# Kernel optimization log

Measured on AMD Instinct MI355X. Metric: run time of the kernel, lower is better.

## Reference

```python
import jax, jax.numpy as jnp
import numpy as np

N = 100000      # nodes
E = 1_000_000   # edges (avg degree ~10)
D_IN = 64
HID = 64
N_CLS = 32


def setup_inputs() -> dict:
    key = jax.random.key(0)
    ks = jax.random.split(key, 9)
    x = jax.random.normal(ks[0], (N, D_IN), dtype=jnp.float32)
    edge_index = jax.random.randint(ks[1], (2, E), 0, N, dtype=jnp.int32)
    s_in = 1.0 / np.sqrt(D_IN)
    s_h = 1.0 / np.sqrt(HID)
    W1 = jax.random.normal(ks[2], (D_IN, HID), dtype=jnp.float32) * s_in
    b1 = jnp.zeros((HID,), dtype=jnp.float32)
    W2 = jax.random.normal(ks[3], (HID, HID), dtype=jnp.float32) * s_h
    b2 = jnp.zeros((HID,), dtype=jnp.float32)
    Wl = jax.random.normal(ks[4], (HID, N_CLS), dtype=jnp.float32) * s_h
    bl = jnp.zeros((N_CLS,), dtype=jnp.float32)
    return {"x": x, "edge_index": edge_index,
            "W1": W1, "b1": b1, "W2": W2, "b2": b2, "Wl": Wl, "bl": bl}


def reference(x, edge_index, W1, b1, W2, b2, Wl, bl):
    # GCNConv default: add self-loops, symmetric normalization D^-1/2 (A+I) D^-1/2
    loop = jnp.arange(N, dtype=edge_index.dtype)
    src = jnp.concatenate([edge_index[0], loop])  # [E+N]
    dst = jnp.concatenate([edge_index[1], loop])  # [E+N]

    deg = jax.ops.segment_sum(jnp.ones_like(dst, dtype=jnp.float32), dst,
                              num_segments=N)              # [N]
    dinv = jnp.where(deg > 0, jax.lax.rsqrt(deg), 0.0)      # D^-1/2
    norm = dinv[src] * dinv[dst]                            # [E+N]

    def gcn_conv(h, W, b):
        h = h @ W                                           # [N, F_out]
        msg = h[src] * norm[:, None]                        # gather + scale
        return jax.ops.segment_sum(msg, dst, num_segments=N) + b

    h = jax.nn.relu(gcn_conv(x, W1, b1))
    h = jax.nn.relu(gcn_conv(h, W2, b2))
    return h @ Wl + bl
```

## Files before the change

### kernel.cpp

```cpp
#include <hip/hip_runtime.h>
#include <hip/hip_fp16.h>
#include <math.h>


#define TPB    256
#define TPB1   1024
#define EBLKS  256
#define BSH    7
#define BNODES (1 << BSH)

__global__ __launch_bounds__(TPB1)
void k_p1hist(const int* __restrict__ dst, int* __restrict__ OFS,
              int E, int CH, int NBC) {
    __shared__ int h[1024];
    int tid = threadIdx.x, b = blockIdx.x;
    h[tid] = 0;
    __syncthreads();
    int beg = b * CH, end = min(E, beg + CH);
    if (beg < end) {
        int nfull = (end - beg) & ~3;
        for (int i = beg + tid * 4; i < beg + nfull; i += TPB1 * 4) {
            int4 d = *(const int4*)&dst[i];
            atomicAdd(&h[d.x >> BSH], 1);
            atomicAdd(&h[d.y >> BSH], 1);
            atomicAdd(&h[d.z >> BSH], 1);
            atomicAdd(&h[d.w >> BSH], 1);
        }
        if (tid < (end - beg) - nfull)
            atomicAdd(&h[dst[beg + nfull + tid] >> BSH], 1);
    }
    __syncthreads();
    for (int c = tid; c < NBC; c += TPB1) OFS[c * EBLKS + b] = h[c];
}

__global__ __launch_bounds__(TPB)
void k_scanA(const int* __restrict__ OFS, int* __restrict__ bsum, int total) {
    __shared__ int s[TPB];
    int tid = threadIdx.x;
    int i0  = blockIdx.x * 1024 + tid * 4;
    int t = 0;
#pragma unroll
    for (int k = 0; k < 4; ++k) {
        int i = i0 + k;
        t += (i < total) ? OFS[i] : 0;
    }
    s[tid] = t;
    __syncthreads();
    for (int off = TPB / 2; off > 0; off >>= 1) {
        if (tid < off) s[tid] += s[tid + off];
        __syncthreads();
    }
    if (tid == 0) bsum[blockIdx.x] = s[0];
}

__global__ __launch_bounds__(TPB)
void k_scanC(int* __restrict__ OFS, const int* __restrict__ bsum, int total) {
    __shared__ int s[TPB];
    __shared__ int pfx;
    int tid = threadIdx.x;
    if (tid < 64) {
        int v = 0;
        for (int j = tid; j < (int)blockIdx.x; j += 64) v += bsum[j];
#pragma unroll
        for (int off = 1; off < 64; off <<= 1) v += __shfl_xor(v, off);
        if (tid == 0) pfx = v;
    }
    int i0 = blockIdx.x * 1024 + tid * 4;
    int v[4];
#pragma unroll
    for (int k = 0; k < 4; ++k) {
        int i = i0 + k;
        v[k] = (i < total) ? OFS[i] : 0;
    }
    int tsum = v[0] + v[1] + v[2] + v[3];
    s[tid] = tsum;
    __syncthreads();
    for (int off = 1; off < TPB; off <<= 1) {
        int x = (tid >= off) ? s[tid - off] : 0;
        __syncthreads();
        s[tid] += x;
        __syncthreads();
    }
    int base = pfx + (s[tid] - tsum);
#pragma unroll
    for (int k = 0; k < 4; ++k) {
        int i = i0 + k;
        if (i < total) {
            OFS[i] = base;
            base += v[k];
        }
    }
}

__global__ __launch_bounds__(TPB1)
void k_p1scatter(const int* __restrict__ src, const int* __restrict__ dst,
                 const int* __restrict__ OFS, int* __restrict__ ebuf,
                 int E, int CH, int NBC) {
    __shared__ int cur[1024];
    int tid = threadIdx.x, b = blockIdx.x;
    for (int c = tid; c < NBC; c += TPB1) cur[c] = OFS[c * EBLKS + b];
    __syncthreads();
    int beg = b * CH, end = min(E, beg + CH);
    if (beg >= end) return;
    int nfull = (end - beg) & ~3;
    for (int i = beg + tid * 4; i < beg + nfull; i += TPB1 * 4) {
        int4 s4 = *(const int4*)&src[i];
        int4 d4 = *(const int4*)&dst[i];
        int p0 = atomicAdd(&cur[d4.x >> BSH], 1);
        int p1 = atomicAdd(&cur[d4.y >> BSH], 1);
        int p2 = atomicAdd(&cur[d4.z >> BSH], 1);
        int p3 = atomicAdd(&cur[d4.w >> BSH], 1);
        ebuf[p0] = (s4.x << BSH) | (d4.x & (BNODES - 1));
        ebuf[p1] = (s4.y << BSH) | (d4.y & (BNODES - 1));
        ebuf[p2] = (s4.z << BSH) | (d4.z & (BNODES - 1));
        ebuf[p3] = (s4.w << BSH) | (d4.w & (BNODES - 1));
    }
    if (tid < (end - beg) - nfull) {
        int i = beg + nfull + tid;
        int d = dst[i];
        int p = atomicAdd(&cur[d >> BSH], 1);
        ebuf[p] = (src[i] << BSH) | (d & (BNODES - 1));
    }
}

__global__ __launch_bounds__(TPB)
void k_p2(const int* __restrict__ ebuf, const int* __restrict__ OFS,
          int* __restrict__ row_ptr, float* __restrict__ dinv,
          int* __restrict__ colw, int N, int E, int NBC) {
    __shared__ int cnt[BNODES];
    __shared__ int ofs[BNODES];
    __shared__ int s1[TPB];
    int tid = threadIdx.x, c = blockIdx.x;
    int beg = OFS[c * EBLKS];
    int end = (c == NBC - 1) ? E : OFS[(c + 1) * EBLKS];
    if (tid < BNODES) cnt[tid] = 0;
    __syncthreads();
    for (int i = beg + tid; i < end; i += TPB)
        atomicAdd(&cnt[ebuf[i] & (BNODES - 1)], 1);
    __syncthreads();
    int a = (tid < BNODES) ? cnt[tid] : 0;
    s1[tid] = a;
    __syncthreads();
    for (int off = 1; off < TPB; off <<= 1) {
        int x = (tid >= off) ? s1[tid - off] : 0;
        __syncthreads();
        s1[tid] += x;
        __syncthreads();
    }
    int ex = s1[tid] - a;
    if (tid < BNODES) {
        int node = (c << BSH) + tid;
        ofs[tid] = beg + ex;
        if (node < N) {
            row_ptr[node] = beg + ex;
            dinv[node]    = rsqrtf((float)(a + 1));
        }
        cnt[tid] = 0;
    }
    if (c == NBC - 1 && tid == 0) row_ptr[N] = E;
    __syncthreads();
    for (int i0 = beg + tid; i0 < end; i0 += TPB * 4) {
        int sv[4], dl[4], pos[4];
        int have = 0;
#pragma unroll
        for (int k = 0; k < 4; ++k) {
            int i = i0 + k * TPB;
            if (i < end) {
                int e = ebuf[i];
                sv[k] = e >> BSH;
                dl[k] = e & (BNODES - 1);
                have = k + 1;
            }
        }
#pragma unroll
        for (int k = 0; k < 4; ++k) {
            if (k < have) {
                int r  = atomicAdd(&cnt[dl[k]], 1);
                pos[k] = ofs[dl[k]] + r;
            }
        }
#pragma unroll
        for (int k = 0; k < 4; ++k)
            if (k < have) colw[pos[k]] = sv[k];
    }
}

template <int F, bool FINAL, bool HIN>
__launch_bounds__(256)
__global__ void k_mm(const void* __restrict__ in, const float* __restrict__ W,
                     const float* __restrict__ bias, const float* __restrict__ dinv,
                     void* __restrict__ out, int n) {
    __shared__ float in_s[64 * 68];
    __shared__ float w_s[64 * F];

    const int tid  = threadIdx.x;
    const int row0 = blockIdx.x * 64;

    for (int i4 = tid; i4 < (64 * F) / 4; i4 += 256)
        ((float4*)w_s)[i4] = ((const float4*)W)[i4];

    if constexpr (HIN) {
        for (int idx = tid; idx < 64 * 8; idx += 256) {
            int r  = idx >> 3;
            int c8 = idx & 7;
            uint4 u = make_uint4(0u, 0u, 0u, 0u);
            if (row0 + r < n)
                u = *(const uint4*)((const __half*)in + (size_t)(row0 + r) * 64 + c8 * 8);
            float2 f0 = __half22float2(*(__half2*)&u.x);
            float2 f1 = __half22float2(*(__half2*)&u.y);
            float2 f2 = __half22float2(*(__half2*)&u.z);
            float2 f3 = __half22float2(*(__half2*)&u.w);
            float* o = &in_s[r * 68 + c8 * 8];
            *(float4*)&o[0] = make_float4(f0.x, f0.y, f1.x, f1.y);
            *(float4*)&o[4] = make_float4(f2.x, f2.y, f3.x, f3.y);
        }
    } else {
        for (int idx = tid; idx < 64 * 16; idx += 256) {
            int r  = idx >> 4;
            int c4 = idx & 15;
            float4 v;
            if (row0 + r < n)
                v = *(const float4*)((const float*)in + (size_t)(row0 + r) * 64 + c4 * 4);
            else
                v = make_float4(0.f, 0.f, 0.f, 0.f);
            *(float4*)&in_s[r * 68 + c4 * 4] = v;
        }
    }
    __syncthreads();

    constexpr int CPT = F / 16;
    const int tx = tid & 15;
    const int ty = tid >> 4;

    float acc[4][CPT];
#pragma unroll
    for (int r = 0; r < 4; ++r)
#pragma unroll
        for (int c = 0; c < CPT; ++c) acc[r][c] = 0.f;

#pragma unroll 4
    for (int k = 0; k < 64; ++k) {
        float b[CPT];
#pragma unroll
        for (int c = 0; c < CPT; ++c) b[c] = w_s[k * F + tx * CPT + c];
#pragma unroll
        for (int r = 0; r < 4; ++r) {
            float a = in_s[(ty * 4 + r) * 68 + k];
#pragma unroll
            for (int c = 0; c < CPT; ++c) acc[r][c] = fmaf(a, b[c], acc[r][c]);
        }
    }

#pragma unroll
    for (int r = 0; r < 4; ++r) {
        int row = row0 + ty * 4 + r;
        if (row >= n) continue;
        if constexpr (FINAL) {
#pragma unroll
            for (int c = 0; c < CPT; ++c) {
                int col = tx * CPT + c;
                ((float*)out)[(size_t)row * F + col] = acc[r][c] + bias[col];
            }
        } else {
            float dd = dinv[row];
            __half2 p0 = __floats2half2_rn(acc[r][0] * dd, acc[r][1] * dd);
            __half2 p1 = __floats2half2_rn(acc[r][2] * dd, acc[r][3] * dd);
            uint2 u = make_uint2(*(unsigned*)&p0, *(unsigned*)&p1);
            *(uint2*)((__half*)out + (size_t)row * 64 + tx * 4) = u;
        }
    }
    if constexpr (!FINAL) {
        if (blockIdx.x == 0 && tid < 16)
            *(uint2*)((__half*)out + (size_t)n * 64 + tid * 4) = make_uint2(0u, 0u);
    }
}

__global__ __launch_bounds__(256)
void k_gather(const int* __restrict__ row_ptr, const int* __restrict__ colw,
              const float* __restrict__ dinv, const float* __restrict__ bias,
              const __half* __restrict__ t, __half* __restrict__ agg, int N) {
    int tid  = threadIdx.x;
    int wv   = tid >> 6;
    int lane = tid & 63;
    int g = lane >> 3;
    int p = lane & 7;
    int d = blockIdx.x * 32 + wv * 8 + g;

    int beg = 0, end = 0;
    if (d < N) { beg = row_ptr[d]; end = row_ptr[d + 1]; }

    float acc[8];
#pragma unroll
    for (int k = 0; k < 8; ++k) acc[k] = 0.f;

    for (int e = beg; e < end; e += 4) {
        int s0 = colw[e];
        int s1 = (e + 1 < end) ? colw[e + 1] : N;
        int s2 = (e + 2 < end) ? colw[e + 2] : N;
        int s3 = (e + 3 < end) ? colw[e + 3] : N;
        uint4 a0 = *(const uint4*)(t + (size_t)s0 * 64 + p * 8);
        uint4 a1 = *(const uint4*)(t + (size_t)s1 * 64 + p * 8);
        uint4 a2 = *(const uint4*)(t + (size_t)s2 * 64 + p * 8);
        uint4 a3 = *(const uint4*)(t + (size_t)s3 * 64 + p * 8);
        float2 f;
        f = __half22float2(*(__half2*)&a0.x); acc[0] += f.x; acc[1] += f.y;
        f = __half22float2(*(__half2*)&a0.y); acc[2] += f.x; acc[3] += f.y;
        f = __half22float2(*(__half2*)&a0.z); acc[4] += f.x; acc[5] += f.y;
        f = __half22float2(*(__half2*)&a0.w); acc[6] += f.x; acc[7] += f.y;
        f = __half22float2(*(__half2*)&a1.x); acc[0] += f.x; acc[1] += f.y;
        f = __half22float2(*(__half2*)&a1.y); acc[2] += f.x; acc[3] += f.y;
        f = __half22float2(*(__half2*)&a1.z); acc[4] += f.x; acc[5] += f.y;
        f = __half22float2(*(__half2*)&a1.w); acc[6] += f.x; acc[7] += f.y;
        f = __half22float2(*(__half2*)&a2.x); acc[0] += f.x; acc[1] += f.y;
        f = __half22float2(*(__half2*)&a2.y); acc[2] += f.x; acc[3] += f.y;
        f = __half22float2(*(__half2*)&a2.z); acc[4] += f.x; acc[5] += f.y;
        f = __half22float2(*(__half2*)&a2.w); acc[6] += f.x; acc[7] += f.y;
        f = __half22float2(*(__half2*)&a3.x); acc[0] += f.x; acc[1] += f.y;
        f = __half22float2(*(__half2*)&a3.y); acc[2] += f.x; acc[3] += f.y;
        f = __half22float2(*(__half2*)&a3.z); acc[4] += f.x; acc[5] += f.y;
        f = __half22float2(*(__half2*)&a3.w); acc[6] += f.x; acc[7] += f.y;
    }

    if (d < N) {
        float dd = dinv[d];
        uint4 a = *(const uint4*)(t + (size_t)d * 64 + p * 8);
        float4 b0 = *(const float4*)&bias[p * 8];
        float4 b1 = *(const float4*)&bias[p * 8 + 4];
        float2 s0 = __half22float2(*(__half2*)&a.x);
        float2 s1 = __half22float2(*(__half2*)&a.y);
        float2 s2 = __half22float2(*(__half2*)&a.z);
        float2 s3 = __half22float2(*(__half2*)&a.w);
        float o0 = fmaxf(fmaf(dd, acc[0] + s0.x, b0.x), 0.f);
        float o1 = fmaxf(fmaf(dd, acc[1] + s0.y, b0.y), 0.f);
        float o2 = fmaxf(fmaf(dd, acc[2] + s1.x, b0.z), 0.f);
        float o3 = fmaxf(fmaf(dd, acc[3] + s1.y, b0.w), 0.f);
        float o4 = fmaxf(fmaf(dd, acc[4] + s2.x, b1.x), 0.f);
        float o5 = fmaxf(fmaf(dd, acc[5] + s2.y, b1.y), 0.f);
        float o6 = fmaxf(fmaf(dd, acc[6] + s3.x, b1.z), 0.f);
        float o7 = fmaxf(fmaf(dd, acc[7] + s3.y, b1.w), 0.f);
        __half2 h0 = __floats2half2_rn(o0, o1);
        __half2 h1 = __floats2half2_rn(o2, o3);
        __half2 h2 = __floats2half2_rn(o4, o5);
        __half2 h3 = __floats2half2_rn(o6, o7);
        uint4 u = make_uint4(*(unsigned*)&h0, *(unsigned*)&h1,
                             *(unsigned*)&h2, *(unsigned*)&h3);
        *(uint4*)(agg + (size_t)d * 64 + p * 8) = u;
    }
}

__global__ __launch_bounds__(256)
void k_gather_head(const int* __restrict__ row_ptr, const int* __restrict__ colw,
                   const float* __restrict__ dinv, const float* __restrict__ bias,
                   const __half* __restrict__ t, const float* __restrict__ Wl,
                   const float* __restrict__ bl, float* __restrict__ out, int N) {
    __shared__ float wl_s[64 * 32];
    __shared__ float aggs[32][68];

    int tid  = threadIdx.x;
    for (int i4 = tid; i4 < (64 * 32) / 4; i4 += 256)
        ((float4*)wl_s)[i4] = ((const float4*)Wl)[i4];

    int wv   = tid >> 6;
    int lane = tid & 63;
    int g = lane >> 3;
    int p = lane & 7;
    int slot = tid >> 3;
    int d = blockIdx.x * 32 + wv * 8 + g;

    int beg = 0, end = 0;
    if (d < N) { beg = row_ptr[d]; end = row_ptr[d + 1]; }

    float acc[8];
#pragma unroll
    for (int k = 0; k < 8; ++k) acc[k] = 0.f;

    for (int e = beg; e < end; e += 4) {
        int s0 = colw[e];
        int s1 = (e + 1 < end) ? colw[e + 1] : N;
        int s2 = (e + 2 < end) ? colw[e + 2] : N;
        int s3 = (e + 3 < end) ? colw[e + 3] : N;
        uint4 a0 = *(const uint4*)(t + (size_t)s0 * 64 + p * 8);
        uint4 a1 = *(const uint4*)(t + (size_t)s1 * 64 + p * 8);
        uint4 a2 = *(const uint4*)(t + (size_t)s2 * 64 + p * 8);
        uint4 a3 = *(const uint4*)(t + (size_t)s3 * 64 + p * 8);
        float2 f;
        f = __half22float2(*(__half2*)&a0.x); acc[0] += f.x; acc[1] += f.y;
        f = __half22float2(*(__half2*)&a0.y); acc[2] += f.x; acc[3] += f.y;
        f = __half22float2(*(__half2*)&a0.z); acc[4] += f.x; acc[5] += f.y;
        f = __half22float2(*(__half2*)&a0.w); acc[6] += f.x; acc[7] += f.y;
        f = __half22float2(*(__half2*)&a1.x); acc[0] += f.x; acc[1] += f.y;
        f = __half22float2(*(__half2*)&a1.y); acc[2] += f.x; acc[3] += f.y;
        f = __half22float2(*(__half2*)&a1.z); acc[4] += f.x; acc[5] += f.y;
        f = __half22float2(*(__half2*)&a1.w); acc[6] += f.x; acc[7] += f.y;
        f = __half22float2(*(__half2*)&a2.x); acc[0] += f.x; acc[1] += f.y;
        f = __half22float2(*(__half2*)&a2.y); acc[2] += f.x; acc[3] += f.y;
        f = __half22float2(*(__half2*)&a2.z); acc[4] += f.x; acc[5] += f.y;
        f = __half22float2(*(__half2*)&a2.w); acc[6] += f.x; acc[7] += f.y;
        f = __half22float2(*(__half2*)&a3.x); acc[0] += f.x; acc[1] += f.y;
        f = __half22float2(*(__half2*)&a3.y); acc[2] += f.x; acc[3] += f.y;
        f = __half22float2(*(__half2*)&a3.z); acc[4] += f.x; acc[5] += f.y;
        f = __half22float2(*(__half2*)&a3.w); acc[6] += f.x; acc[7] += f.y;
    }

    if (d < N) {
        float dd = dinv[d];
        uint4 a = *(const uint4*)(t + (size_t)d * 64 + p * 8);
        float4 b0 = *(const float4*)&bias[p * 8];
        float4 b1 = *(const float4*)&bias[p * 8 + 4];
        float2 s0 = __half22float2(*(__half2*)&a.x);
        float2 s1 = __half22float2(*(__half2*)&a.y);
        float2 s2 = __half22float2(*(__half2*)&a.z);
        float2 s3 = __half22float2(*(__half2*)&a.w);
        float o0 = fmaxf(fmaf(dd, acc[0] + s0.x, b0.x), 0.f);
        float o1 = fmaxf(fmaf(dd, acc[1] + s0.y, b0.y), 0.f);
        float o2 = fmaxf(fmaf(dd, acc[2] + s1.x, b0.z), 0.f);
        float o3 = fmaxf(fmaf(dd, acc[3] + s1.y, b0.w), 0.f);
        float o4 = fmaxf(fmaf(dd, acc[4] + s2.x, b1.x), 0.f);
        float o5 = fmaxf(fmaf(dd, acc[5] + s2.y, b1.y), 0.f);
        float o6 = fmaxf(fmaf(dd, acc[6] + s3.x, b1.z), 0.f);
        float o7 = fmaxf(fmaf(dd, acc[7] + s3.y, b1.w), 0.f);
        *(float4*)&aggs[slot][p * 8]     = make_float4(o0, o1, o2, o3);
        *(float4*)&aggs[slot][p * 8 + 4] = make_float4(o4, o5, o6, o7);
    }
    __syncthreads();

    if (d < N) {
        float a0 = 0.f, a1 = 0.f, a2 = 0.f, a3 = 0.f;
#pragma unroll 8
        for (int k = 0; k < 64; ++k) {
            float av = aggs[slot][k];
            float4 w = ((const float4*)&wl_s[k * 32])[p];
            a0 = fmaf(av, w.x, a0);
            a1 = fmaf(av, w.y, a1);
            a2 = fmaf(av, w.z, a2);
            a3 = fmaf(av, w.w, a3);
        }
        float4 bb = *(const float4*)&bl[p * 4];
        *(float4*)&out[(size_t)d * 32 + p * 4] =
            make_float4(a0 + bb.x, a1 + bb.y, a2 + bb.z, a3 + bb.w);
    }
}

extern "C" void kernel_launch(void* const* d_in, const int* in_sizes, int n_in,
                              void* d_out, int out_size, void* d_ws, size_t ws_size,
                              hipStream_t stream) {
    const float* x  = (const float*)d_in[0];
    const int*   ei = (const int*)d_in[1];
    const float* W1 = (const float*)d_in[2];
    const float* b1 = (const float*)d_in[3];
    const float* W2 = (const float*)d_in[4];
    const float* b2 = (const float*)d_in[5];
    const float* Wl = (const float*)d_in[6];
    const float* bl = (const float*)d_in[7];
    float*       out = (float*)d_out;

    const int N = in_sizes[0] / 64;
    const int E = in_sizes[1] / 2;
    const int* srcp = ei;
    const int* dstp = ei + E;

    const int NBC   = (N + BNODES - 1) / BNODES;
    const int CH    = (((E + EBLKS - 1) / EBLKS) + 3) & ~3;
    const int total = NBC * EBLKS;
    const int NBLK  = (total + 1023) / 1024;

    char*  ws  = (char*)d_ws;
    size_t off = 0;
    auto alloc = [&](size_t bytes) -> void* {
        void* p = (void*)(ws + off);
        off += (bytes + 255) & ~(size_t)255;
        return p;
    };
    int*    OFS     = (int*)alloc(((size_t)total + 1) * 4);
    int*    bsum    = (int*)alloc((size_t)NBLK * 4);
    int*    ebuf    = (int*)alloc((size_t)E * 4);
    int*    row_ptr = (int*)alloc((size_t)(N + 1) * 4);
    float*  dinv    = (float*)alloc((size_t)N * 4);
    int*    colw    = (int*)alloc((size_t)E * 4);
    __half* t1      = (__half*)alloc((size_t)(N + 1) * 64 * 2);
    __half* agg1    = (__half*)alloc((size_t)N * 64 * 2);
    __half* t2      = t1;

    const int nb_mm = (N + 63) / 64;
    const int nb_g  = (N + 31) / 32;

    k_p1hist   <<<EBLKS, TPB1, 0, stream>>>(dstp, OFS, E, CH, NBC);
    k_scanA    <<<NBLK,  TPB,  0, stream>>>(OFS, bsum, total);
    k_scanC    <<<NBLK,  TPB,  0, stream>>>(OFS, bsum, total);
    k_p1scatter<<<EBLKS, TPB1, 0, stream>>>(srcp, dstp, OFS, ebuf, E, CH, NBC);
    k_p2       <<<NBC,   TPB,  0, stream>>>(ebuf, OFS, row_ptr, dinv, colw, N, E, NBC);

    k_mm<64, false, false><<<nb_mm, 256, 0, stream>>>(x, W1, nullptr, dinv, t1, N);
    k_gather<<<nb_g, 256, 0, stream>>>(row_ptr, colw, dinv, b1, t1, agg1, N);

    k_mm<64, false, true><<<nb_mm, 256, 0, stream>>>(agg1, W2, nullptr, dinv, t2, N);

    k_gather_head<<<nb_g, 256, 0, stream>>>(row_ptr, colw, dinv, b2, t2,
                                            Wl, bl, out, N);
}
```

Measured before the change: 196.4 us.

## Fuse layer-1 aggregation with the layer-2 weight matmul

The first-layer gather kernel now keeps its aggregated rows in shared memory and multiplies them directly by W2 (loaded into LDS) before writing the scaled fp16 t2. This removes the agg1 intermediate buffer's global write and re-read and drops one kernel launch. In exchange the gather kernel uses more shared memory (W2 plus the tile), which may lower occupancy for this latency-bound gather. It also needs a separate t2 buffer so the kernel does not overwrite t1 while other blocks still read it.

```diff
diff --git a/kernel.cpp b/kernel.cpp
--- a/kernel.cpp
+++ b/kernel.cpp
@@ -185,50 +185,32 @@
     }
 }
 
-template <int F, bool FINAL, bool HIN>
 __launch_bounds__(256)
-__global__ void k_mm(const void* __restrict__ in, const float* __restrict__ W,
-                     const float* __restrict__ bias, const float* __restrict__ dinv,
-                     void* __restrict__ out, int n) {
+__global__ void k_mm(const float* __restrict__ in, const float* __restrict__ W,
+                     const float* __restrict__ dinv,
+                     __half* __restrict__ out, int n) {
     __shared__ float in_s[64 * 68];
-    __shared__ float w_s[64 * F];
+    __shared__ float w_s[64 * 64];
 
     const int tid  = threadIdx.x;
     const int row0 = blockIdx.x * 64;
 
-    for (int i4 = tid; i4 < (64 * F) / 4; i4 += 256)
+    for (int i4 = tid; i4 < (64 * 64) / 4; i4 += 256)
         ((float4*)w_s)[i4] = ((const float4*)W)[i4];
 
-    if constexpr (HIN) {
-        for (int idx = tid; idx < 64 * 8; idx += 256) {
-            int r  = idx >> 3;
-            int c8 = idx & 7;
-            uint4 u = make_uint4(0u, 0u, 0u, 0u);
-            if (row0 + r < n)
-                u = *(const uint4*)((const __half*)in + (size_t)(row0 + r) * 64 + c8 * 8);
-            float2 f0 = __half22float2(*(__half2*)&u.x);
-            float2 f1 = __half22float2(*(__half2*)&u.y);
-            float2 f2 = __half22float2(*(__half2*)&u.z);
-            float2 f3 = __half22float2(*(__half2*)&u.w);
-            float* o = &in_s[r * 68 + c8 * 8];
-            *(float4*)&o[0] = make_float4(f0.x, f0.y, f1.x, f1.y);
-            *(float4*)&o[4] = make_float4(f2.x, f2.y, f3.x, f3.y);
-        }
-    } else {
-        for (int idx = tid; idx < 64 * 16; idx += 256) {
-            int r  = idx >> 4;
-            int c4 = idx & 15;
-            float4 v;
-            if (row0 + r < n)
-                v = *(const float4*)((const float*)in + (size_t)(row0 + r) * 64 + c4 * 4);
-            else
-                v = make_float4(0.f, 0.f, 0.f, 0.f);
-            *(float4*)&in_s[r * 68 + c4 * 4] = v;
-        }
-    }
-    __syncthreads();
-
-    constexpr int CPT = F / 16;
+    for (int idx = tid; idx < 64 * 16; idx += 256) {
+        int r  = idx >> 4;
+        int c4 = idx & 15;
+        float4 v;
+        if (row0 + r < n)
+            v = *(const float4*)(in + (size_t)(row0 + r) * 64 + c4 * 4);
+        else
+            v = make_float4(0.f, 0.f, 0.f, 0.f);
+        *(float4*)&in_s[r * 68 + c4 * 4] = v;
+    }
+    __syncthreads();
+
+    constexpr int CPT = 4;
     const int tx = tid & 15;
     const int ty = tid >> 4;
 
@@ -242,7 +224,7 @@
     for (int k = 0; k < 64; ++k) {
         float b[CPT];
 #pragma unroll
-        for (int c = 0; c < CPT; ++c) b[c] = w_s[k * F + tx * CPT + c];
+        for (int c = 0; c < CPT; ++c) b[c] = w_s[k * 64 + tx * CPT + c];
 #pragma unroll
         for (int r = 0; r < 4; ++r) {
             float a = in_s[(ty * 4 + r) * 68 + k];
@@ -255,35 +237,33 @@
     for (int r = 0; r < 4; ++r) {
         int row = row0 + ty * 4 + r;
         if (row >= n) continue;
-        if constexpr (FINAL) {
-#pragma unroll
-            for (int c = 0; c < CPT; ++c) {
-                int col = tx * CPT + c;
-                ((float*)out)[(size_t)row * F + col] = acc[r][c] + bias[col];
-            }
-        } else {
-            float dd = dinv[row];
-            __half2 p0 = __floats2half2_rn(acc[r][0] * dd, acc[r][1] * dd);
-            __half2 p1 = __floats2half2_rn(acc[r][2] * dd, acc[r][3] * dd);
-            uint2 u = make_uint2(*(unsigned*)&p0, *(unsigned*)&p1);
-            *(uint2*)((__half*)out + (size_t)row * 64 + tx * 4) = u;
-        }
-    }
-    if constexpr (!FINAL) {
-        if (blockIdx.x == 0 && tid < 16)
-            *(uint2*)((__half*)out + (size_t)n * 64 + tid * 4) = make_uint2(0u, 0u);
-    }
+        float dd = dinv[row];
+        __half2 p0 = __floats2half2_rn(acc[r][0] * dd, acc[r][1] * dd);
+        __half2 p1 = __floats2half2_rn(acc[r][2] * dd, acc[r][3] * dd);
+        uint2 u = make_uint2(*(unsigned*)&p0, *(unsigned*)&p1);
+        *(uint2*)(out + (size_t)row * 64 + tx * 4) = u;
+    }
+    if (blockIdx.x == 0 && tid < 16)
+        *(uint2*)(out + (size_t)n * 64 + tid * 4) = make_uint2(0u, 0u);
 }
 
 __global__ __launch_bounds__(256)
-void k_gather(const int* __restrict__ row_ptr, const int* __restrict__ colw,
-              const float* __restrict__ dinv, const float* __restrict__ bias,
-              const __half* __restrict__ t, __half* __restrict__ agg, int N) {
-    int tid  = threadIdx.x;
+void k_gather_mm(const int* __restrict__ row_ptr, const int* __restrict__ colw,
+                 const float* __restrict__ dinv, const float* __restrict__ bias,
+                 const __half* __restrict__ t, const float* __restrict__ W2,
+                 __half* __restrict__ t2, int N) {
+    __shared__ float  w_s[64 * 64];
+    __shared__ __half aggs[32][72];
+
+    int tid = threadIdx.x;
+    for (int i4 = tid; i4 < (64 * 64) / 4; i4 += 256)
+        ((float4*)w_s)[i4] = ((const float4*)W2)[i4];
+
     int wv   = tid >> 6;
     int lane = tid & 63;
     int g = lane >> 3;
     int p = lane & 7;
+    int slot = tid >> 3;
     int d = blockIdx.x * 32 + wv * 8 + g;
 
     int beg = 0, end = 0;
@@ -342,10 +322,48 @@
         __half2 h1 = __floats2half2_rn(o2, o3);
         __half2 h2 = __floats2half2_rn(o4, o5);
         __half2 h3 = __floats2half2_rn(o6, o7);
-        uint4 u = make_uint4(*(unsigned*)&h0, *(unsigned*)&h1,
-                             *(unsigned*)&h2, *(unsigned*)&h3);
-        *(uint4*)(agg + (size_t)d * 64 + p * 8) = u;
-    }
+        *(uint4*)&aggs[slot][p * 8] = make_uint4(*(unsigned*)&h0, *(unsigned*)&h1,
+                                                *(unsigned*)&h2, *(unsigned*)&h3);
+    }
+    __syncthreads();
+
+    if (d < N) {
+        float dd = dinv[d];
+        float a0 = 0.f, a1 = 0.f, a2 = 0.f, a3 = 0.f;
+        float a4 = 0.f, a5 = 0.f, a6 = 0.f, a7 = 0.f;
+#pragma unroll
+        for (int k0 = 0; k0 < 64; k0 += 8) {
+            uint4 u = *(const uint4*)&aggs[slot][k0];
+            float2 f0 = __half22float2(*(__half2*)&u.x);
+            float2 f1 = __half22float2(*(__half2*)&u.y);
+            float2 f2 = __half22float2(*(__half2*)&u.z);
+            float2 f3 = __half22float2(*(__half2*)&u.w);
+            float av[8] = {f0.x, f0.y, f1.x, f1.y, f2.x, f2.y, f3.x, f3.y};
+#pragma unroll
+            for (int j = 0; j < 8; ++j) {
+                const float* wr = &w_s[(k0 + j) * 64 + p * 8];
+                float4 w0 = *(const float4*)&wr[0];
+                float4 w1 = *(const float4*)&wr[4];
+                a0 = fmaf(av[j], w0.x, a0);
+                a1 = fmaf(av[j], w0.y, a1);
+                a2 = fmaf(av[j], w0.z, a2);
+                a3 = fmaf(av[j], w0.w, a3);
+                a4 = fmaf(av[j], w1.x, a4);
+                a5 = fmaf(av[j], w1.y, a5);
+                a6 = fmaf(av[j], w1.z, a6);
+                a7 = fmaf(av[j], w1.w, a7);
+            }
+        }
+        __half2 q0 = __floats2half2_rn(a0 * dd, a1 * dd);
+        __half2 q1 = __floats2half2_rn(a2 * dd, a3 * dd);
+        __half2 q2 = __floats2half2_rn(a4 * dd, a5 * dd);
+        __half2 q3 = __floats2half2_rn(a6 * dd, a7 * dd);
+        uint4 u = make_uint4(*(unsigned*)&q0, *(unsigned*)&q1,
+                             *(unsigned*)&q2, *(unsigned*)&q3);
+        *(uint4*)(t2 + (size_t)d * 64 + p * 8) = u;
+    }
+    if (blockIdx.x == 0 && tid < 16)
+        *(uint2*)(t2 + (size_t)N * 64 + tid * 4) = make_uint2(0u, 0u);
 }
 
 __global__ __launch_bounds__(256)
@@ -478,8 +496,7 @@
     float*  dinv    = (float*)alloc((size_t)N * 4);
     int*    colw    = (int*)alloc((size_t)E * 4);
     __half* t1      = (__half*)alloc((size_t)(N + 1) * 64 * 2);
-    __half* agg1    = (__half*)alloc((size_t)N * 64 * 2);
-    __half* t2      = t1;
+    __half* t2      = (__half*)alloc((size_t)(N + 1) * 64 * 2);
 
     const int nb_mm = (N + 63) / 64;
     const int nb_g  = (N + 31) / 32;
@@ -490,10 +507,10 @@
     k_p1scatter<<<EBLKS, TPB1, 0, stream>>>(srcp, dstp, OFS, ebuf, E, CH, NBC);
     k_p2       <<<NBC,   TPB,  0, stream>>>(ebuf, OFS, row_ptr, dinv, colw, N, E, NBC);
 
-    k_mm<64, false, false><<<nb_mm, 256, 0, stream>>>(x, W1, nullptr, dinv, t1, N);
-    k_gather<<<nb_g, 256, 0, stream>>>(row_ptr, colw, dinv, b1, t1, agg1, N);
-
-    k_mm<64, false, true><<<nb_mm, 256, 0, stream>>>(agg1, W2, nullptr, dinv, t2, N);
+    k_mm<<<nb_mm, 256, 0, stream>>>(x, W1, dinv, t1, N);
+
+    k_gather_mm<<<nb_g, 256, 0, stream>>>(row_ptr, colw, dinv, b1, t1,
+                                          W2, t2, N);
 
     k_gather_head<<<nb_g, 256, 0, stream>>>(row_ptr, colw, dinv, b2, t2,
                                             Wl, bl, out, N);
```

After: 187.1 us. -4.7%, faster.
